# Optimization experiments

Measured on AMD Instinct MI355X. Metric: run time of the kernel, lower is better.

Reference implementation:

```python
import jax, jax.numpy as jnp
import numpy as np

S, B, E, H = 192, 2, 512, 2
D = E // H      # head_dim = 256 == E/2; required so attn_fc(3*D) matches concat of three E/2 chunks
BH = B * H

def _lin(x, W, b):
    return x @ W.T + b

def setup_inputs():
    key = jax.random.key(0)
    ks = jax.random.split(key, 16)
    p = lambda k, *s: jax.random.normal(k, s, jnp.float32) * 0.02
    return {
        "query":       jax.random.normal(ks[0], (S, B, E), jnp.float32),
        "entity":      jax.random.normal(ks[1], (S, B, E), jnp.float32),
        "ex_entity":   jax.random.normal(ks[2], (S, B, B, E), jnp.float32),
        "ex_relation": jax.random.normal(ks[3], (S, B, B, E), jnp.float32),
        "Wq": p(ks[4], D, E), "bq": jnp.zeros((D,), jnp.float32),
        "Wk": p(ks[5], D, E), "bk": jnp.zeros((D,), jnp.float32),
        "Wv": p(ks[6], D, E), "bv": jnp.zeros((D,), jnp.float32),
        "We": p(ks[7], D, E), "be": jnp.zeros((D,), jnp.float32),
        "Wxe": p(ks[8], D, E), "bxe": jnp.zeros((D,), jnp.float32),
        "Wxr": p(ks[9], D, E), "bxr": jnp.zeros((D,), jnp.float32),
        "Wa": p(ks[10], 1, 3 * D), "ba": jnp.zeros((1,), jnp.float32),
        "Wo": p(ks[11], E, E), "bo": jnp.zeros((E,), jnp.float32),
    }

def reference(query, entity, ex_entity, ex_relation,
              Wq, bq, Wk, bk, Wv, bv, We, be, Wxe, bxe, Wxr, bxr, Wa, ba, Wo, bo):
    e = _lin(entity, We, be)            # [S,B,D]
    q = _lin(query, Wq, bq)             # [S,B,D]
    exr = _lin(ex_entity, Wxe, bxe)     # exent_proj(ex_entity) -> [S,B,B,D]
    exe = _lin(ex_relation, Wxr, bxr)   # exrel_proj(ex_relation) -> [S,B,B,D]
    e_b = jnp.broadcast_to(e[:, :, None, :], exe.shape)
    exz = jnp.concatenate([exe, e_b, exr], axis=-1)                              # [S,B,B,3D]
    exw = jax.nn.softmax(jax.nn.leaky_relu((exz @ Wa.T + ba)[..., 0]), axis=-1)  # [S,B,B]
    we = jnp.einsum('sbk,skd->sbd', exw, e)  # torch.bmm; dead when en_tgt==tgt (faithful fwd compute)
    del we
    qe = jnp.concatenate([q, e], axis=-1)    # [S,B,E]  (else-branch: e.size(0)==q.size(0))
    k = _lin(query, Wk, bk)
    v = _lin(query, Wv, bv)
    ke = jnp.concatenate([k, e], axis=-1)
    ve = jnp.concatenate([v, e], axis=-1)
    shp = lambda x: jnp.swapaxes(x.reshape(S, BH, D), 0, 1)  # torch _shape -> [BH,S,D]
    qe_s, ke_s, ve_s = shp(qe), shp(ke), shp(ve)
    # edge[i,j,b,:] = entity[i,b] - entity[j,b]; torch then does a flat .view(BH,S,S,D)
    edge = (entity[:, None] - entity[None, :]).reshape(BH, S, S, D)
    # qe: transpose(0,1).repeat(S,1,1,1).transpose(0,1).reshape -> broadcast over src then flat reshape
    qe_r = jnp.broadcast_to(jnp.swapaxes(qe_s, 0, 1)[:, None], (S, S, BH, D)).reshape(BH, S, S, D)
    # ke: repeat(S,1,1,1).reshape (flat)
    ke_r = jnp.broadcast_to(ke_s[None], (S, BH, S, D)).reshape(BH, S, S, D)
    z = jnp.concatenate([qe_r, ke_r, edge], axis=-1)                             # [BH,S,S,3D]
    aw = jax.nn.softmax(jax.nn.leaky_relu((z @ Wa.T + ba)[..., 0]), axis=-1)     # [BH,S,S]
    out = jnp.einsum('bts,bsd->btd', aw, ve_s)                                   # [BH,S,D]
    out = jnp.swapaxes(out, 0, 1).reshape(S, B, E)
    return _lin(out, Wo, bo)
```

## Files before the change

kernel.cpp:

```cpp
#include <hip/hip_runtime.h>
#include <math.h>


#define SS 192
#define WTO 262144
#define TO  524288
#define VO  526592
#define EO  624896
#define OO  723200

__device__ __forceinline__ float wave_reduce_add(float p) {
    #pragma unroll
    for (int off = 32; off >= 1; off >>= 1) p += __shfl_xor(p, off, 64);
    return p;
}

__global__ __launch_bounds__(1024) void k_projprep(
    const float* __restrict__ query, const float* __restrict__ entity,
    const float* __restrict__ Wq, const float* __restrict__ bq,
    const float* __restrict__ Wk, const float* __restrict__ bk,
    const float* __restrict__ Wv, const float* __restrict__ bv,
    const float* __restrict__ We, const float* __restrict__ be,
    const float* __restrict__ Wa, const float* __restrict__ Wo,
    float* __restrict__ ws)
{
    __shared__ __align__(16) float shb[8448];
    __shared__ __align__(16) float uo[516];
    int blk = blockIdx.x;
    int tid = threadIdx.x;
    int wv   = __builtin_amdgcn_readfirstlane(tid >> 6);
    int lane = tid & 63;

    if (blk < 192) {
        int m   = blk / 96;
        int rem = blk % 96;
        int dh  = rem / 48;
        int rg  = rem % 48;
        int r0  = rg * 8;
        int d0  = dh * 128;
        int q   = __builtin_amdgcn_readfirstlane(tid >> 7);
        int dl  = tid & 127;
        const float4* Wsrc = (const float4*)(m ? We : Wv);
        const float*  bias = m ? be : bv;
        const float*  A    = m ? entity : query;
        float*        dst  = ws + (m ? EO : VO);
        const float4* A4   = (const float4*)A;
        float4* WL = (float4*)shb;

        float acc[8];
        #pragma unroll
        for (int r = 0; r < 8; r++) acc[r] = 0.f;

        for (int c = 0; c < 8; c++) {
            #pragma unroll
            for (int j = 0; j < 2; j++) {
                int idx  = tid + j * 1024;
                int dloc = idx >> 4;
                int k4l  = idx & 15;
                WL[k4l * 129 + dloc] =
                    Wsrc[(size_t)(d0 + dloc) * 128 + c * 16 + k4l];
            }
            __syncthreads();
            #pragma unroll
            for (int j = 0; j < 2; j++) {
                int k4l = q * 2 + j;
                float4 w = WL[k4l * 129 + dl];
                int k4 = c * 16 + k4l;
                #pragma unroll
                for (int r = 0; r < 8; r++) {
                    float4 a = A4[(size_t)(r0 + r) * 128 + k4];
                    acc[r] += a.x * w.x + a.y * w.y + a.z * w.z + a.w * w.w;
                }
            }
            __syncthreads();
        }
        float* part = shb;
        #pragma unroll
        for (int r = 0; r < 8; r++) part[q * 1024 + r * 128 + dl] = acc[r];
        __syncthreads();
        {
            int r = tid >> 7, d2 = tid & 127;
            float v = 0.f;
            #pragma unroll
            for (int k = 0; k < 8; k++) v += part[k * 1024 + r * 128 + d2];
            dst[(size_t)(r0 + r) * 256 + d0 + d2] = v + bias[d0 + d2];
        }
        return;
    }

    if (blk < 256) {
        int o  = (blk - 192) * 1024 + tid;
        int c  = o >> 7;
        int k4 = o & 127;
        ((float4*)(ws + WTO))[k4 * 512 + c] = ((const float4*)Wo)[o];
        return;
    }

    if (blk < 264) {
        float* red = shb;
        int tab = blk - 256;
        int p   = (tab < 4) ? tab : tab - 4;
        int b   = p >> 1, h = p & 1;
        const float* wa   = Wa + ((tab < 4) ? 0 : 256);
        const float* W    = h ? We : ((tab < 4) ? Wq : Wk);
        const float* bias = h ? be : ((tab < 4) ? bq : bk);
        const float* x    = h ? entity : query;

        float u8[8];
        #pragma unroll
        for (int i = 0; i < 8; i++) u8[i] = 0.f;
        #pragma unroll 4
        for (int dd = 0; dd < 16; dd++) {
            int d = wv * 16 + dd;
            float wad = wa[d];
            const float4* Wr = (const float4*)(W + (size_t)d * 512);
            float4 w0 = Wr[lane * 2], w1 = Wr[lane * 2 + 1];
            u8[0] += wad * w0.x; u8[1] += wad * w0.y; u8[2] += wad * w0.z; u8[3] += wad * w0.w;
            u8[4] += wad * w1.x; u8[5] += wad * w1.y; u8[6] += wad * w1.z; u8[7] += wad * w1.w;
        }
        if (wv < 8) {
            #pragma unroll
            for (int i = 0; i < 8; i++) red[wv * 512 + lane * 8 + i] = u8[i];
        }
        __syncthreads();
        if (wv >= 8) {
            #pragma unroll
            for (int i = 0; i < 8; i++)
                atomicAdd(&red[(wv - 8) * 512 + lane * 8 + i], u8[i]);
        }
        __syncthreads();
        if (tid < 512) {
            float s = 0.f;
            #pragma unroll
            for (int w = 0; w < 8; w++) s += red[w * 512 + tid];
            uo[tid] = s;
        }
        __syncthreads();
        if (tid < 256) red[tid] = wa[tid] * bias[tid];
        __syncthreads();
        for (int o = 128; o >= 1; o >>= 1) {
            if (tid < o) red[tid] += red[tid + o];
            __syncthreads();
        }
        float off = red[0];

        const float4* u4 = (const float4*)uo;
        float4 ua = u4[lane * 2], ub = u4[lane * 2 + 1];
        for (int rr = 0; rr < 12; rr++) {
            int r = wv * 12 + rr;
            const float4* xr = (const float4*)(x + (size_t)(r * 2 + b) * 512);
            float4 a0 = xr[lane * 2], a1 = xr[lane * 2 + 1];
            float pp = a0.x*ua.x + a0.y*ua.y + a0.z*ua.z + a0.w*ua.w
                     + a1.x*ub.x + a1.y*ub.y + a1.z*ub.z + a1.w*ub.w;
            pp = wave_reduce_add(pp);
            if (lane == 0) ws[TO + tab * SS + r] = pp + off;
        }
        return;
    }

    {
        int m = blk - 264;
        float4 wa4 = ((const float4*)(Wa + 512))[lane];
        for (int rr = 0; rr < 12; rr++) {
            int i = wv * 12 + rr;
            const float4* er = (const float4*)(entity
                + (size_t)(i * 2 + (m >> 1)) * 512 + (m & 1) * 256);
            float4 e4 = er[lane];
            float pp = e4.x*wa4.x + e4.y*wa4.y + e4.z*wa4.z + e4.w*wa4.w;
            pp = wave_reduce_add(pp);
            if (lane == 0) ws[TO + (8 + m) * SS + i] = pp;
        }
    }
}

__global__ __launch_bounds__(1024) void k_attn(
    const float* __restrict__ ba_p, float* __restrict__ ws)
{
    __shared__ __align__(16) float pl[4096];
    __shared__ __align__(16) float sp4[768];
    int blk = blockIdx.x;
    int bh  = blk & 3;
    int rem2 = blk >> 2;
    int tg  = rem2 % 48;
    int dhf = rem2 / 48;
    int b = bh >> 1, h = bh & 1;
    const float* T = ws + TO;
    float ba = ba_p[0];
    int tid  = threadIdx.x;
    int wv   = __builtin_amdgcn_readfirstlane(tid >> 6);
    int lane = tid & 63;

    if (wv < 4) {
        int ti = wv;
        int i_idx = bh * 48 + tg;
        float sc[3]; float mx = -1e30f;
        #pragma unroll
        for (int i = 0; i < 3; i++) {
            int s_ = lane + 64 * i;
            int m  = s_ & 3;
            int j  = ti * 48 + (s_ >> 2);
            float xv = T[m * SS + i_idx] + T[(4 + ti) * SS + s_]
                     + T[(8 + m) * SS + i_idx] - T[(8 + m) * SS + j] + ba;
            xv = (xv >= 0.f) ? xv : 0.01f * xv;
            sc[i] = xv; mx = fmaxf(mx, xv);
        }
        #pragma unroll
        for (int o = 32; o >= 1; o >>= 1) mx = fmaxf(mx, __shfl_xor(mx, o, 64));
        float sum = 0.f;
        #pragma unroll
        for (int i = 0; i < 3; i++) { sc[i] = __expf(sc[i] - mx); sum += sc[i]; }
        sum = wave_reduce_add(sum);
        float inv = 1.f / sum;
        #pragma unroll
        for (int i = 0; i < 3; i++) sp4[ti * SS + lane + 64 * i] = sc[i] * inv;
    }
    __syncthreads();

    int sq = __builtin_amdgcn_readfirstlane(tid >> 7);
    int dl = tid & 127;
    int dd = dhf * 128 + dl;
    const float* src = ws + (h ? EO : VO) + b * 256 + dd;
    float a[4] = {0.f, 0.f, 0.f, 0.f};
    int s0 = sq * 24;
    #pragma unroll 8
    for (int s2 = 0; s2 < 24; s2++) {
        int s = s0 + s2;
        float xv = src[(size_t)s * 512];
        #pragma unroll
        for (int ti = 0; ti < 4; ti++) a[ti] += sp4[ti * SS + s] * xv;
    }
    #pragma unroll
    for (int ti = 0; ti < 4; ti++) pl[sq * 512 + ti * 128 + dl] = a[ti];
    __syncthreads();
    if (tid < 512) {
        int ti = tid >> 7, d2 = tid & 127;
        float v = 0.f;
        #pragma unroll
        for (int k = 0; k < 8; k++) v += pl[k * 512 + ti * 128 + d2];
        int t = tg * 4 + ti;
        ws[OO + (size_t)(2 * t + b) * 512 + h * 256 + dhf * 128 + d2] = v;
    }
}

__global__ __launch_bounds__(1024) void k_out(
    const float* __restrict__ bo, const float* __restrict__ ws,
    float* __restrict__ out)
{
    __shared__ float pl[4096];
    int blk = blockIdx.x;
    int rg  = blk >> 2;
    int cg  = blk & 3;
    int r0  = rg * 4;
    int c0  = cg * 128;
    int tid = threadIdx.x;
    int kc  = __builtin_amdgcn_readfirstlane(tid >> 7);
    int cl  = tid & 127;
    const float4* A4 = (const float4*)(ws + OO);
    const float4* WT = (const float4*)(ws + WTO);

    float acc[4];
    #pragma unroll
    for (int r = 0; r < 4; r++) acc[r] = 0.f;

    int k4b = kc * 16;
    #pragma unroll 8
    for (int i = 0; i < 16; i++) {
        int k4 = k4b + i;
        float4 w = WT[(size_t)k4 * 512 + c0 + cl];
        #pragma unroll
        for (int r = 0; r < 4; r++) {
            float4 a = A4[(r0 + r) * 128 + k4];
            acc[r] += a.x * w.x + a.y * w.y + a.z * w.z + a.w * w.w;
        }
    }
    #pragma unroll
    for (int r = 0; r < 4; r++) pl[kc * 512 + r * 128 + cl] = acc[r];
    __syncthreads();
    if (tid < 512) {
        int r = tid >> 7, c2 = tid & 127;
        float v = 0.f;
        #pragma unroll
        for (int k = 0; k < 8; k++) v += pl[k * 512 + r * 128 + c2];
        out[(size_t)(r0 + r) * 512 + c0 + c2] = v + bo[c0 + c2];
    }
}

extern "C" void kernel_launch(void* const* d_in, const int* in_sizes, int n_in,
                              void* d_out, int out_size, void* d_ws, size_t ws_size,
                              hipStream_t stream) {
    const float* query  = (const float*)d_in[0];
    const float* entity = (const float*)d_in[1];
    const float* Wq = (const float*)d_in[4];  const float* bq = (const float*)d_in[5];
    const float* Wk = (const float*)d_in[6];  const float* bk = (const float*)d_in[7];
    const float* Wv = (const float*)d_in[8];  const float* bv = (const float*)d_in[9];
    const float* We = (const float*)d_in[10]; const float* be = (const float*)d_in[11];
    const float* Wa = (const float*)d_in[16]; const float* ba = (const float*)d_in[17];
    const float* Wo = (const float*)d_in[18]; const float* bo = (const float*)d_in[19];
    float* ws  = (float*)d_ws;
    float* out = (float*)d_out;

    hipLaunchKernelGGL(k_projprep, dim3(268), dim3(1024), 0, stream,
                       query, entity, Wq, bq, Wk, bk, Wv, bv, We, be, Wa, Wo, ws);
    hipLaunchKernelGGL(k_attn, dim3(384), dim3(1024), 0, stream, ba, ws);
    hipLaunchKernelGGL(k_out,  dim3(384), dim3(1024), 0, stream, bo, ws, out);
}
```

Before: 40.23 us.

## Fuse attention aggregation and output projection into one kernel

Merges the attention-weighted sum and the output linear layer into a single kernel with 192 blocks. Each block now computes both heads for one batch and four targets, writes the four attention rows to a per-block scratch area in global memory, and then multiplies them by the transposed Wo for half the output columns. This removes one kernel launch and the grid-wide dependency between attention and projection. In exchange there are fewer blocks, more work per block, and a global write then read within the block that relies on a barrier plus a scalar cache invalidate for visibility, and each block's reads of the WT matrix are duplicated across target groups.

```diff
diff --git a/kernel.cpp b/kernel.cpp
--- a/kernel.cpp
+++ b/kernel.cpp
@@ -7,7 +7,7 @@
 #define TO  524288
 #define VO  526592
 #define EO  624896
-#define OO  723200
+#define ROWS 723200
 
 __device__ __forceinline__ float wave_reduce_add(float p) {
     #pragma unroll
@@ -173,25 +173,26 @@
     }
 }
 
-__global__ __launch_bounds__(1024) void k_attn(
-    const float* __restrict__ ba_p, float* __restrict__ ws)
+__global__ __launch_bounds__(1024) void k_attnout(
+    const float* __restrict__ ba_p, const float* __restrict__ bo,
+    float* __restrict__ ws, float* __restrict__ out)
 {
-    __shared__ __align__(16) float pl[4096];
-    __shared__ __align__(16) float sp4[768];
+    __shared__ __align__(16) float spT[SS * 8];
+    __shared__ __align__(16) float pu[8192];
     int blk = blockIdx.x;
-    int bh  = blk & 3;
-    int rem2 = blk >> 2;
-    int tg  = rem2 % 48;
-    int dhf = rem2 / 48;
-    int b = bh >> 1, h = bh & 1;
+    int b   = blk / 96;
+    int rem = blk % 96;
+    int tg  = rem >> 1;
+    int cg  = rem & 1;
+    int tid  = threadIdx.x;
+    int wvi  = __builtin_amdgcn_readfirstlane(tid >> 6);
+    int lane = tid & 63;
     const float* T = ws + TO;
     float ba = ba_p[0];
-    int tid  = threadIdx.x;
-    int wv   = __builtin_amdgcn_readfirstlane(tid >> 6);
-    int lane = tid & 63;
-
-    if (wv < 4) {
-        int ti = wv;
+
+    if (wvi < 8) {
+        int h = wvi >> 2, ti = wvi & 3;
+        int bh = 2 * b + h;
         int i_idx = bh * 48 + tg;
         float sc[3]; float mx = -1e30f;
         #pragma unroll
@@ -212,76 +213,85 @@
         sum = wave_reduce_add(sum);
         float inv = 1.f / sum;
         #pragma unroll
-        for (int i = 0; i < 3; i++) sp4[ti * SS + lane + 64 * i] = sc[i] * inv;
+        for (int i = 0; i < 3; i++)
+            spT[(lane + 64 * i) * 8 + h * 4 + ti] = sc[i] * inv;
     }
     __syncthreads();
 
-    int sq = __builtin_amdgcn_readfirstlane(tid >> 7);
-    int dl = tid & 127;
-    int dd = dhf * 128 + dl;
-    const float* src = ws + (h ? EO : VO) + b * 256 + dd;
-    float a[4] = {0.f, 0.f, 0.f, 0.f};
-    int s0 = sq * 24;
-    #pragma unroll 8
-    for (int s2 = 0; s2 < 24; s2++) {
-        int s = s0 + s2;
-        float xv = src[(size_t)s * 512];
-        #pragma unroll
-        for (int ti = 0; ti < 4; ti++) a[ti] += sp4[ti * SS + s] * xv;
-    }
-    #pragma unroll
-    for (int ti = 0; ti < 4; ti++) pl[sq * 512 + ti * 128 + dl] = a[ti];
+    {
+        int h  = __builtin_amdgcn_readfirstlane(tid >> 9);
+        int sq = __builtin_amdgcn_readfirstlane((tid >> 7) & 3);
+        int d2 = tid & 127;
+        const float2* src2 = (const float2*)(ws + (h ? EO : VO));
+        const float4* spT4 = (const float4*)spT;
+        float2 acc2[4];
+        #pragma unroll
+        for (int ti = 0; ti < 4; ti++) acc2[ti] = make_float2(0.f, 0.f);
+        int s0 = sq * 48;
+        #pragma unroll 8
+        for (int s2 = 0; s2 < 48; s2++) {
+            int s = s0 + s2;
+            float4 p4 = spT4[s * 2 + h];
+            float2 v  = src2[(size_t)(s * 2 + b) * 128 + d2];
+            acc2[0].x += p4.x * v.x; acc2[0].y += p4.x * v.y;
+            acc2[1].x += p4.y * v.x; acc2[1].y += p4.y * v.y;
+            acc2[2].x += p4.z * v.x; acc2[2].y += p4.z * v.y;
+            acc2[3].x += p4.w * v.x; acc2[3].y += p4.w * v.y;
+        }
+        float2* pf2 = (float2*)pu;
+        #pragma unroll
+        for (int ti = 0; ti < 4; ti++)
+            pf2[((h * 4 + sq) * 4 + ti) * 128 + d2] = acc2[ti];
+    }
     __syncthreads();
-    if (tid < 512) {
-        int ti = tid >> 7, d2 = tid & 127;
-        float v = 0.f;
-        #pragma unroll
-        for (int k = 0; k < 8; k++) v += pl[k * 512 + ti * 128 + d2];
-        int t = tg * 4 + ti;
-        ws[OO + (size_t)(2 * t + b) * 512 + h * 256 + dhf * 128 + d2] = v;
-    }
-}
-
-__global__ __launch_bounds__(1024) void k_out(
-    const float* __restrict__ bo, const float* __restrict__ ws,
-    float* __restrict__ out)
-{
-    __shared__ float pl[4096];
-    int blk = blockIdx.x;
-    int rg  = blk >> 2;
-    int cg  = blk & 3;
-    int r0  = rg * 4;
-    int c0  = cg * 128;
-    int tid = threadIdx.x;
-    int kc  = __builtin_amdgcn_readfirstlane(tid >> 7);
-    int cl  = tid & 127;
-    const float4* A4 = (const float4*)(ws + OO);
-    const float4* WT = (const float4*)(ws + WTO);
-
-    float acc[4];
-    #pragma unroll
-    for (int r = 0; r < 4; r++) acc[r] = 0.f;
-
-    int k4b = kc * 16;
-    #pragma unroll 8
-    for (int i = 0; i < 16; i++) {
-        int k4 = k4b + i;
-        float4 w = WT[(size_t)k4 * 512 + c0 + cl];
-        #pragma unroll
-        for (int r = 0; r < 4; r++) {
-            float4 a = A4[(r0 + r) * 128 + k4];
-            acc[r] += a.x * w.x + a.y * w.y + a.z * w.z + a.w * w.w;
-        }
-    }
-    #pragma unroll
-    for (int r = 0; r < 4; r++) pl[kc * 512 + r * 128 + cl] = acc[r];
+
+    {
+        const float* partf = pu;
+        int ti = tid >> 8, dd = tid & 255;
+        float r0 = 0.f, r1 = 0.f;
+        #pragma unroll
+        for (int sq = 0; sq < 4; sq++) {
+            r0 += partf[((0 + sq) * 4 + ti) * 256 + dd];
+            r1 += partf[((4 + sq) * 4 + ti) * 256 + dd];
+        }
+        float* wsrows = ws + ROWS + blk * 2048;
+        wsrows[ti * 512 + dd]       = r0;
+        wsrows[ti * 512 + 256 + dd] = r1;
+    }
     __syncthreads();
-    if (tid < 512) {
-        int r = tid >> 7, c2 = tid & 127;
-        float v = 0.f;
-        #pragma unroll
-        for (int k = 0; k < 8; k++) v += pl[k * 512 + r * 128 + c2];
-        out[(size_t)(r0 + r) * 512 + c0 + c2] = v + bo[c0 + c2];
+    asm volatile("s_dcache_inv" ::: "memory");
+
+    {
+        int kc = __builtin_amdgcn_readfirstlane(tid >> 8);
+        int cl = tid & 255;
+        int c0 = cg * 256;
+        const float4* rows4 = (const float4*)(ws + ROWS + blk * 2048);
+        const float4* WT    = (const float4*)(ws + WTO);
+        float acc[4];
+        #pragma unroll
+        for (int r = 0; r < 4; r++) acc[r] = 0.f;
+        int k4b = kc * 32;
+        #pragma unroll 8
+        for (int i = 0; i < 32; i++) {
+            int k4 = k4b + i;
+            float4 w = WT[(size_t)k4 * 512 + c0 + cl];
+            #pragma unroll
+            for (int r = 0; r < 4; r++) {
+                float4 a = rows4[r * 128 + k4];
+                acc[r] += a.x * w.x + a.y * w.y + a.z * w.z + a.w * w.w;
+            }
+        }
+        #pragma unroll
+        for (int r = 0; r < 4; r++) pu[kc * 1024 + r * 256 + cl] = acc[r];
+    }
+    __syncthreads();
+    {
+        int r = tid >> 8, cl = tid & 255;
+        int c = cg * 256 + cl;
+        float v = pu[r * 256 + cl] + pu[1024 + r * 256 + cl]
+                + pu[2048 + r * 256 + cl] + pu[3072 + r * 256 + cl];
+        int t = tg * 4 + r;
+        out[(size_t)(2 * t + b) * 512 + c] = v + bo[c];
     }
 }
 
@@ -301,6 +311,6 @@
 
     hipLaunchKernelGGL(k_projprep, dim3(268), dim3(1024), 0, stream,
                        query, entity, Wq, bq, Wk, bk, Wv, bv, We, be, Wa, Wo, ws);
-    hipLaunchKernelGGL(k_attn, dim3(384), dim3(1024), 0, stream, ba, ws);
-    hipLaunchKernelGGL(k_out,  dim3(384), dim3(1024), 0, stream, bo, ws, out);
+    hipLaunchKernelGGL(k_attnout, dim3(192), dim3(1024), 0, stream,
+                       ba, bo, ws, out);
 }
```

New measurement: 51.96 us. +29.1%, slower.
